# Optimization experiments

Hardware: AMD Instinct MI355X
Metric: run time of the kernel (lower is better)

The kernel has to match this reference:

```python
import jax, jax.numpy as jnp
import numpy as np
import math

B, L, D = 2, 4096, 1024
K = D // 4


def _rotor(angles):
    # angles: [..., 6] -> scalar part s: [...], bivector part: [..., 6]
    mag = jnp.maximum(jnp.linalg.norm(angles, axis=-1), 1e-8)
    s = jnp.cos(mag)
    biv = (jnp.sin(mag) / mag)[..., None] * angles
    return s, biv


def _apply_rotor(s, biv, v):
    # s: [...], biv: [..., 6] (e12,e13,e14,e23,e24,e34), v: [..., 4]
    t12, t13, t14, t23, t24, t34 = (biv[..., i] for i in range(6))
    v1, v2, v3, v4 = (v[..., i] for i in range(4))
    s2 = s * s
    ts = 2.0 * s
    v1n = v1 * (s2 - t12 * t12 - t13 * t13 - t14 * t14) + ts * (v2 * t12 + v3 * t13 + v4 * t14)
    v2n = v2 * (s2 - t12 * t12 - t23 * t23 - t24 * t24) + ts * (-v1 * t12 + v3 * t23 + v4 * t24)
    v3n = v3 * (s2 - t13 * t13 - t23 * t23 - t34 * t34) + ts * (-v1 * t13 - v2 * t23 + v4 * t34)
    v4n = v4 * (s2 - t14 * t14 - t24 * t24 - t34 * t34) + ts * (-v1 * t14 - v2 * t24 - v3 * t34)
    return jnp.stack([v1n, v2n, v3n, v4n], axis=-1)


def _forward(x, wk1, bk1, wk2, bk2, wq1, bq1, wq2, bq2, wv, bv, ln_g, ln_b, wo, bo):
    b, l, d = x.shape
    k = d // 4
    gelu = lambda t: jax.nn.gelu(t, approximate=False)  # torch nn.GELU default = exact
    half_pi = math.pi / 2
    key_angles = (jnp.tanh(gelu(x @ wk1 + bk1) @ wk2 + bk2) * half_pi).reshape(b, l, k, 6)
    query_angles = (jnp.tanh(gelu(x @ wq1 + bq1) @ wq2 + bq2) * half_pi).reshape(b, l, k, 6)
    value = (x @ wv + bv).reshape(b, l, k, 4)
    ks, kb = _rotor(key_angles)
    qs, qb = _rotor(query_angles)
    rotated_value = _apply_rotor(ks, kb, value)          # [B,L,K,4]
    memory = jnp.cumsum(rotated_value, axis=1)            # running sum over sequence
    retrieved = _apply_rotor(qs, -qb, memory)             # reversed query rotor
    retrieved = retrieved.reshape(b, l, d)
    norm = jnp.sqrt(jnp.arange(1, l + 1, dtype=x.dtype))[None, :, None]
    r = retrieved / norm
    # LayerNorm (eps=1e-5) then Linear
    mu = jnp.mean(r, axis=-1, keepdims=True)
    var = jnp.mean((r - mu) ** 2, axis=-1, keepdims=True)
    rn = (r - mu) / jnp.sqrt(var + 1e-5) * ln_g + ln_b
    return x + rn @ wo + bo


def setup_inputs() -> dict:
    key = jax.random.key(0)
    ks = jax.random.split(key, 8)
    lin = lambda k, fi, fo: (jax.random.normal(k, (fi, fo), jnp.float32) * 0.02)
    return {
        "x": jax.random.normal(ks[0], (B, L, D), jnp.float32),
        "wk1": lin(ks[1], D, D), "bk1": jnp.zeros((D,), jnp.float32),
        "wk2": lin(ks[2], D, K * 6), "bk2": jnp.zeros((K * 6,), jnp.float32),
        "wq1": lin(ks[3], D, D), "bq1": jnp.zeros((D,), jnp.float32),
        "wq2": lin(ks[4], D, K * 6), "bq2": jnp.zeros((K * 6,), jnp.float32),
        "wv": lin(ks[5], D, D), "bv": jnp.zeros((D,), jnp.float32),
        "ln_g": jnp.ones((D,), jnp.float32), "ln_b": jnp.zeros((D,), jnp.float32),
        "wo": lin(ks[6], D, D), "bo": jnp.zeros((D,), jnp.float32),
    }


def reference(x, wk1, bk1, wk2, bk2, wq1, bq1, wq2, bq2, wv, bv, ln_g, ln_b, wo, bo):
    return _forward(x, wk1, bk1, wk2, bk2, wq1, bq1, wq2, bq2, wv, bv, ln_g, ln_b, wo, bo)
```

## Files before the change

kernel.cpp:

```cpp
#include <hip/hip_runtime.h>
#include <hip/hip_bf16.h>
#include <math.h>

#define D_DIM 1024
#define L_DIM 4096
#define B_DIM 2
#define K_DIM 256
#define N6    1536
#define M_ROWS 8192
#define CHUNKS 256
#define CHUNK_LEN 16
#define HALF_PI 1.57079632679489662f

typedef __attribute__((ext_vector_type(8))) short short8;
typedef __attribute__((ext_vector_type(4))) float f32x4;
typedef unsigned short us;

__device__ __forceinline__ void gload_lds16(const void* g, void* l) {
    __builtin_amdgcn_global_load_lds(
        (const __attribute__((address_space(1))) unsigned int*)g,
        (__attribute__((address_space(3))) unsigned int*)l,
        16, 0, 0);
}
__device__ __forceinline__ float bf2f(us u) {
    union { unsigned int i; float f; } c; c.i = ((unsigned int)u) << 16; return c.f;
}
__device__ __forceinline__ us f2bf(float v) {
    __hip_bfloat16 h = __float2bfloat16(v);
    return *(us*)&h;
}
__device__ __forceinline__ float tanh_fast(float x) {
    return 1.0f - 2.0f / (1.0f + __expf(2.0f * x));
}
__device__ __forceinline__ float gelu_fast(float x) {
    return x / (1.0f + __expf(-1.5957691216057308f * x * (1.0f + 0.044715f * x * x)));
}

__device__ __forceinline__ void rotor_from_angles(const float a[6], float& s, float b[6]) {
    float m2 = a[0]*a[0] + a[1]*a[1] + a[2]*a[2] + a[3]*a[3] + a[4]*a[4] + a[5]*a[5];
    float mag = fmaxf(sqrtf(m2), 1e-8f);
    s = __cosf(mag);
    float f = __sinf(mag) / mag;
    #pragma unroll
    for (int i = 0; i < 6; ++i) b[i] = f * a[i];
}
__device__ __forceinline__ void apply_rotor(float s, const float b[6], const float v[4], float o[4]) {
    float t12 = b[0], t13 = b[1], t14 = b[2], t23 = b[3], t24 = b[4], t34 = b[5];
    float v1 = v[0], v2 = v[1], v3 = v[2], v4 = v[3];
    float s2 = s * s;
    float ts = 2.0f * s;
    o[0] = v1 * (s2 - t12*t12 - t13*t13 - t14*t14) + ts * ( v2*t12 + v3*t13 + v4*t14);
    o[1] = v2 * (s2 - t12*t12 - t23*t23 - t24*t24) + ts * (-v1*t12 + v3*t23 + v4*t24);
    o[2] = v3 * (s2 - t13*t13 - t23*t23 - t34*t34) + ts * (-v1*t13 - v2*t23 + v4*t34);
    o[3] = v4 * (s2 - t14*t14 - t24*t24 - t34*t34) + ts * (-v1*t14 - v2*t24 - v3*t34);
}

__global__ __launch_bounds__(256)
void pack_b4(const float* __restrict__ w0, const float* __restrict__ w1,
             const float* __restrict__ w2, const float* __restrict__ w3,
             us* __restrict__ o0, us* __restrict__ o1,
             us* __restrict__ o2, us* __restrict__ o3, int Kd, int N)
{
    const float* W = (blockIdx.z == 0) ? w0 : (blockIdx.z == 1) ? w1 : (blockIdx.z == 2) ? w2 : w3;
    us* O = (blockIdx.z == 0) ? o0 : (blockIdx.z == 1) ? o1 : (blockIdx.z == 2) ? o2 : o3;
    if (W == nullptr) return;
    int nf = blockIdx.x;
    int kt = blockIdx.y * 4 + (threadIdx.x >> 6);
    int l = threadIdx.x & 63;
    int n = nf * 16 + (l & 15);
    int k0 = kt * 32 + (l >> 4) * 8;
    union { us u[8]; uint4 v; } pk;
    #pragma unroll
    for (int j = 0; j < 8; ++j)
        pk.u[j] = f2bf(W[(size_t)(k0 + j) * N + n]);
    *(uint4*)(O + ((size_t)nf * (Kd >> 5) + kt) * 512 + l * 8) = pk.v;
}

__global__ __launch_bounds__(256)
void cvt_bf16_kernel(const float* __restrict__ in, us* __restrict__ out)
{
    size_t i = ((size_t)blockIdx.x * 256 + threadIdx.x) * 8;
    float4 v0 = *(const float4*)(in + i);
    float4 v1 = *(const float4*)(in + i + 4);
    union { us u[8]; uint4 v; } pk;
    pk.u[0] = f2bf(v0.x); pk.u[1] = f2bf(v0.y); pk.u[2] = f2bf(v0.z); pk.u[3] = f2bf(v0.w);
    pk.u[4] = f2bf(v1.x); pk.u[5] = f2bf(v1.y); pk.u[6] = f2bf(v1.z); pk.u[7] = f2bf(v1.w);
    *(uint4*)(out + i) = pk.v;
}

__device__ __forceinline__ int xcd_swz(int bid, int nwg) {
    int cpx = nwg >> 3;
    return (bid & 7) * cpx + (bid >> 3);
}


#define GBAR()  do { __builtin_amdgcn_s_barrier(); __builtin_amdgcn_sched_barrier(0); } while (0)

__device__ __forceinline__ void gemm128_core(
    const us* __restrict__ Ab, const us* __restrict__ Bp, int Kd, int bn,
    short* lds, f32x4 (&acc)[4][4])
{
    const int tid = threadIdx.x;
    const int l = tid & 63, w = tid >> 6;
    const int wr = w >> 1, wc = w & 1;
    const int fr = l & 15, fq = l >> 4;
    const int nkt = Kd >> 5;

    #pragma unroll
    for (int i = 0; i < 4; ++i)
        #pragma unroll
        for (int j = 0; j < 4; ++j)
            acc[i][j] = (f32x4){0.f, 0.f, 0.f, 0.f};

    const us* bptr[4];
    #pragma unroll
    for (int ni = 0; ni < 4; ++ni)
        bptr[ni] = Bp + ((size_t)((bn >> 4) + wc * 4 + ni) * nkt) * 512 + l * 8;

    const int sr = tid >> 2, su = tid & 3;
    const int slu = su ^ ((sr >> 1) & 3);
    const us* gA0 = Ab + (size_t)sr * Kd + slu * 8;
    const us* gA1 = gA0 + (size_t)64 * Kd;

    const int swu = (fq ^ ((fr >> 1) & 3)) * 8;
    const int arow = (wr * 64 + fr) * 32 + swu;

    gload_lds16(gA0,      lds + tid * 8);
    gload_lds16(gA1,      lds + 2048 + tid * 8);
    gload_lds16(gA0 + 32, lds + 4096 + tid * 8);
    gload_lds16(gA1 + 32, lds + 6144 + tid * 8);
    gload_lds16(gA0 + 64, lds + 8192 + tid * 8);
    gload_lds16(gA1 + 64, lds + 10240 + tid * 8);
    short8 bcur[4], bnxt[4];
    #pragma unroll
    for (int ni = 0; ni < 4; ++ni)
        bcur[ni] = *(const short8*)(bptr[ni]);
    asm volatile("s_waitcnt vmcnt(8)" ::: "memory");
    GBAR();

    #pragma unroll 2
    for (int t = 0; t < nkt; ++t) {
        const int cb = (t % 3) * 4096;
        const int sb = ((t + 2) % 3) * 4096;
        const int ka = ((t + 2) < nkt ? (t + 2) : (nkt - 1)) * 32;
        const int kb = ((t + 1) < nkt ? (t + 1) : (nkt - 1));

        #pragma unroll
        for (int ni = 0; ni < 4; ++ni)
            bnxt[ni] = *(const short8*)(bptr[ni] + (size_t)kb * 512);
        gload_lds16(gA0 + ka, lds + sb + tid * 8);
        gload_lds16(gA1 + ka, lds + sb + 2048 + tid * 8);

        short8 a[4];
        #pragma unroll
        for (int mi = 0; mi < 4; ++mi)
            a[mi] = *(const short8*)(lds + cb + arow + mi * 512);

        __builtin_amdgcn_s_setprio(1);
        #pragma unroll
        for (int mi = 0; mi < 4; ++mi)
            #pragma unroll
            for (int ni = 0; ni < 4; ++ni)
                acc[mi][ni] = __builtin_amdgcn_mfma_f32_16x16x32_bf16(bcur[ni], a[mi], acc[mi][ni], 0, 0, 0);
        __builtin_amdgcn_sched_barrier(0);
        __builtin_amdgcn_s_setprio(0);

        #pragma unroll
        for (int ni = 0; ni < 4; ++ni)
            bcur[ni] = bnxt[ni];

        asm volatile("s_waitcnt vmcnt(6)" ::: "memory");
        GBAR();
    }
}

__global__ __launch_bounds__(256, 3)
void gemm_fused3(const us* __restrict__ xb,
                 const us* __restrict__ w0p, const us* __restrict__ w1p, const us* __restrict__ w2p,
                 const float* __restrict__ b0, const float* __restrict__ b1, const float* __restrict__ b2,
                 us* __restrict__ o0, us* __restrict__ o1, us* __restrict__ o2)
{
    __shared__ short lds[12288];
    const int wg = xcd_swz(blockIdx.x, 1536);
    const int bm = (wg / 24) * 128;
    const int col = wg % 24;
    const int r = col >> 3;
    const int bn = (col & 7) * 128;
    const us* Bp = (r == 0) ? w0p : (r == 1) ? w1p : w2p;
    const float* bias = (r == 0) ? b0 : (r == 1) ? b1 : b2;
    us* outp = (r == 0) ? o0 : (r == 1) ? o1 : o2;
    f32x4 acc[4][4];
    gemm128_core(xb + (size_t)bm * D_DIM, Bp, D_DIM, bn, lds, acc);
    const int l = threadIdx.x & 63, w = threadIdx.x >> 6;
    const int wr = w >> 1, wc = w & 1, fr = l & 15, fq = l >> 4;
    #pragma unroll
    for (int mi = 0; mi < 4; ++mi) {
        int row = bm + wr * 64 + mi * 16 + fr;
        #pragma unroll
        for (int ni = 0; ni < 4; ++ni) {
            int c0 = bn + wc * 64 + ni * 16 + fq * 4;
            float4 bs = *(const float4*)(bias + c0);
            float v0 = acc[mi][ni][0] + bs.x, v1 = acc[mi][ni][1] + bs.y;
            float v2 = acc[mi][ni][2] + bs.z, v3 = acc[mi][ni][3] + bs.w;
            if (r < 2) { v0 = gelu_fast(v0); v1 = gelu_fast(v1); v2 = gelu_fast(v2); v3 = gelu_fast(v3); }
            ushort4 pk; pk.x = f2bf(v0); pk.y = f2bf(v1); pk.z = f2bf(v2); pk.w = f2bf(v3);
            *(ushort4*)(outp + (size_t)row * D_DIM + c0) = pk;
        }
    }
}

__global__ __launch_bounds__(256, 3)
void gemm_angles(const us* __restrict__ Hk, const us* __restrict__ Hq,
                 const us* __restrict__ wk2p, const us* __restrict__ wq2p,
                 const float* __restrict__ bk2, const float* __restrict__ bq2,
                 us* __restrict__ ak, us* __restrict__ aq)
{
    __shared__ short lds[12288];
    const int wg = xcd_swz(blockIdx.x, 1536);
    const int z = wg / 768;
    const int rem = wg % 768;
    const int bm = (rem / 12) * 128;
    const int bn = (rem % 12) * 128;
    const us* A  = z ? Hq : Hk;
    const us* Bp = z ? wq2p : wk2p;
    const float* bias = z ? bq2 : bk2;
    us* outp = z ? aq : ak;
    f32x4 acc[4][4];
    gemm128_core(A + (size_t)bm * D_DIM, Bp, D_DIM, bn, lds, acc);
    const int l = threadIdx.x & 63, w = threadIdx.x >> 6;
    const int wr = w >> 1, wc = w & 1, fr = l & 15, fq = l >> 4;
    #pragma unroll
    for (int mi = 0; mi < 4; ++mi) {
        int row = bm + wr * 64 + mi * 16 + fr;
        #pragma unroll
        for (int ni = 0; ni < 4; ++ni) {
            int c0 = bn + wc * 64 + ni * 16 + fq * 4;
            float4 bs = *(const float4*)(bias + c0);
            ushort4 pk;
            pk.x = f2bf(tanh_fast(acc[mi][ni][0] + bs.x) * HALF_PI);
            pk.y = f2bf(tanh_fast(acc[mi][ni][1] + bs.y) * HALF_PI);
            pk.z = f2bf(tanh_fast(acc[mi][ni][2] + bs.z) * HALF_PI);
            pk.w = f2bf(tanh_fast(acc[mi][ni][3] + bs.w) * HALF_PI);
            *(ushort4*)(outp + (size_t)row * N6 + c0) = pk;
        }
    }
}

__global__ __launch_bounds__(256, 3)
void gemm_final(const us* __restrict__ rn, const us* __restrict__ wop,
                const float* __restrict__ bo, const float* __restrict__ x,
                float* __restrict__ out)
{
    __shared__ short lds[12288];
    const int wg = xcd_swz(blockIdx.x, 512);
    const int bm = (wg / 8) * 128;
    const int bn = (wg % 8) * 128;
    f32x4 acc[4][4];
    gemm128_core(rn + (size_t)bm * D_DIM, wop, D_DIM, bn, lds, acc);
    const int l = threadIdx.x & 63, w = threadIdx.x >> 6;
    const int wr = w >> 1, wc = w & 1, fr = l & 15, fq = l >> 4;
    #pragma unroll
    for (int mi = 0; mi < 4; ++mi) {
        int row = bm + wr * 64 + mi * 16 + fr;
        #pragma unroll
        for (int ni = 0; ni < 4; ++ni) {
            int c0 = bn + wc * 64 + ni * 16 + fq * 4;
            size_t off = (size_t)row * D_DIM + c0;
            float4 bs = *(const float4*)(bo + c0);
            float4 rx = *(const float4*)(x + off);
            float4 o;
            o.x = acc[mi][ni][0] + bs.x + rx.x;
            o.y = acc[mi][ni][1] + bs.y + rx.y;
            o.z = acc[mi][ni][2] + bs.z + rx.z;
            o.w = acc[mi][ni][3] + bs.w + rx.w;
            *(float4*)(out + off) = o;
        }
    }
}

__global__ __launch_bounds__(256)
void rot_chunk_sum(const us* __restrict__ value, const us* __restrict__ ak,
                   float4* __restrict__ sums)
{
    int bc = blockIdx.x;
    int b = bc >> 8, c = bc & 255;
    int k = threadIdx.x;
    float4 acc = make_float4(0.f, 0.f, 0.f, 0.f);
    size_t row0 = (size_t)b * L_DIM + c * CHUNK_LEN;
    for (int i = 0; i < CHUNK_LEN; ++i) {
        size_t row = row0 + i;
        ushort4 uv = *(const ushort4*)(value + row * D_DIM + k * 4);
        const unsigned int* ap = (const unsigned int*)(ak + row * N6 + k * 6);
        unsigned int a0 = ap[0], a1 = ap[1], a2 = ap[2];
        float a[6] = { bf2f(a0 & 0xffff), bf2f(a0 >> 16), bf2f(a1 & 0xffff),
                       bf2f(a1 >> 16), bf2f(a2 & 0xffff), bf2f(a2 >> 16) };
        float s, bb[6];
        rotor_from_angles(a, s, bb);
        float v[4] = {bf2f(uv.x), bf2f(uv.y), bf2f(uv.z), bf2f(uv.w)}, o[4];
        apply_rotor(s, bb, v, o);
        acc.x += o[0]; acc.y += o[1]; acc.z += o[2]; acc.w += o[3];
    }
    sums[(size_t)bc * 256 + k] = acc;
}

__global__ __launch_bounds__(256)
void scan_chunks_kernel(const float4* __restrict__ sums, float4* __restrict__ carry)
{
    int b = blockIdx.x >> 8;
    int k = blockIdx.x & 255;
    int c = threadIdx.x;
    __shared__ float4 sh[CHUNKS];
    float4 v = sums[((size_t)(b * CHUNKS + c)) * 256 + k];
    sh[c] = v;
    __syncthreads();
    for (int off = 1; off < CHUNKS; off <<= 1) {
        float4 t = make_float4(0.f, 0.f, 0.f, 0.f);
        if (c >= off) t = sh[c - off];
        __syncthreads();
        v.x += t.x; v.y += t.y; v.z += t.z; v.w += t.w;
        sh[c] = v;
        __syncthreads();
    }
    float4 ex = make_float4(0.f, 0.f, 0.f, 0.f);
    if (c > 0) ex = sh[c - 1];
    carry[((size_t)(b * CHUNKS + c)) * 256 + k] = ex;
}

__global__ __launch_bounds__(256)
void scan_apply_ln(const us* __restrict__ value, const us* __restrict__ ak,
                   const us* __restrict__ aq, const float4* __restrict__ carry,
                   const float* __restrict__ g, const float* __restrict__ bta,
                   us* __restrict__ rn)
{
    int bc = blockIdx.x;
    int b = bc >> 8, c = bc & 255;
    int k = threadIdx.x;
    int wv = k >> 6, lane = k & 63;
    float4 run = carry[(size_t)bc * 256 + k];
    float4 gv = *(const float4*)(g + k * 4);
    float4 bv = *(const float4*)(bta + k * 4);
    __shared__ float reds[4], redq[4];
    for (int i = 0; i < CHUNK_LEN; ++i) {
        int l = c * CHUNK_LEN + i;
        size_t row = (size_t)b * L_DIM + l;
        ushort4 uv = *(const ushort4*)(value + row * D_DIM + k * 4);
        const unsigned int* akp = (const unsigned int*)(ak + row * N6 + k * 6);
        unsigned int ka0 = akp[0], ka1 = akp[1], ka2 = akp[2];
        float a[6] = { bf2f(ka0 & 0xffff), bf2f(ka0 >> 16), bf2f(ka1 & 0xffff),
                       bf2f(ka1 >> 16), bf2f(ka2 & 0xffff), bf2f(ka2 >> 16) };
        float s, bb[6];
        rotor_from_angles(a, s, bb);
        float v[4] = {bf2f(uv.x), bf2f(uv.y), bf2f(uv.z), bf2f(uv.w)}, o[4];
        apply_rotor(s, bb, v, o);
        run.x += o[0]; run.y += o[1]; run.z += o[2]; run.w += o[3];
        const unsigned int* aqp = (const unsigned int*)(aq + row * N6 + k * 6);
        unsigned int qa0 = aqp[0], qa1 = aqp[1], qa2 = aqp[2];
        float aq6[6] = { bf2f(qa0 & 0xffff), bf2f(qa0 >> 16), bf2f(qa1 & 0xffff),
                         bf2f(qa1 >> 16), bf2f(qa2 & 0xffff), bf2f(qa2 >> 16) };
        float qs, qb[6];
        rotor_from_angles(aq6, qs, qb);
        #pragma unroll
        for (int t = 0; t < 6; ++t) qb[t] = -qb[t];
        float mem[4] = {run.x, run.y, run.z, run.w}, o2[4];
        apply_rotor(qs, qb, mem, o2);
        float inv = rsqrtf((float)(l + 1));
        o2[0] *= inv; o2[1] *= inv; o2[2] *= inv; o2[3] *= inv;
        float sm = o2[0] + o2[1] + o2[2] + o2[3];
        float qm = o2[0]*o2[0] + o2[1]*o2[1] + o2[2]*o2[2] + o2[3]*o2[3];
        #pragma unroll
        for (int off = 1; off < 64; off <<= 1) {
            sm += __shfl_xor(sm, off);
            qm += __shfl_xor(qm, off);
        }
        if (lane == 0) { reds[wv] = sm; redq[wv] = qm; }
        __syncthreads();
        sm = reds[0] + reds[1] + reds[2] + reds[3];
        qm = redq[0] + redq[1] + redq[2] + redq[3];
        float mu = sm * (1.0f / 1024.0f);
        float var = qm * (1.0f / 1024.0f) - mu * mu;
        float rstd = rsqrtf(var + 1e-5f);
        ushort4 pk;
        pk.x = f2bf((o2[0] - mu) * rstd * gv.x + bv.x);
        pk.y = f2bf((o2[1] - mu) * rstd * gv.y + bv.y);
        pk.z = f2bf((o2[2] - mu) * rstd * gv.z + bv.z);
        pk.w = f2bf((o2[3] - mu) * rstd * gv.w + bv.w);
        *(ushort4*)(rn + row * D_DIM + k * 4) = pk;
        __syncthreads();
    }
}

extern "C" void kernel_launch(void* const* d_in, const int* in_sizes, int n_in,
                              void* d_out, int out_size, void* d_ws, size_t ws_size,
                              hipStream_t stream)
{
    const float* x   = (const float*)d_in[0];
    const float* wk1 = (const float*)d_in[1];
    const float* bk1 = (const float*)d_in[2];
    const float* wk2 = (const float*)d_in[3];
    const float* bk2 = (const float*)d_in[4];
    const float* wq1 = (const float*)d_in[5];
    const float* bq1 = (const float*)d_in[6];
    const float* wq2 = (const float*)d_in[7];
    const float* bq2 = (const float*)d_in[8];
    const float* wv  = (const float*)d_in[9];
    const float* bv  = (const float*)d_in[10];
    const float* lng = (const float*)d_in[11];
    const float* lnb = (const float*)d_in[12];
    const float* wo  = (const float*)d_in[13];
    const float* bo  = (const float*)d_in[14];
    float* out = (float*)d_out;

    char* ws = (char*)d_ws;
    us* xb    = (us*)(ws);
    us* Hk    = (us*)(ws + (16ull  << 20));
    us* Hq    = (us*)(ws + (32ull  << 20));
    us* val   = (us*)(ws + (48ull  << 20));
    us* ak    = (us*)(ws + (64ull  << 20));
    us* aq    = (us*)(ws + (88ull  << 20));
    float4* sums  = (float4*)(ws + (112ull << 20));
    float4* carry = (float4*)(ws + (114ull << 20));
    us* wk1p  = (us*)(ws + (116ull << 20));
    us* wq1p  = (us*)(ws + (118ull << 20));
    us* wvp   = (us*)(ws + (120ull << 20));
    us* wop   = (us*)(ws + (122ull << 20));
    us* wk2p  = (us*)(ws + (124ull << 20));
    us* wq2p  = (us*)(ws + (127ull << 20));
    us* rn    = xb;

    dim3 blk(256);
    pack_b4<<<dim3(D_DIM / 16, D_DIM / 128, 4), blk, 0, stream>>>(
        wk1, wq1, wv, wo, wk1p, wq1p, wvp, wop, D_DIM, D_DIM);
    pack_b4<<<dim3(N6 / 16, D_DIM / 128, 2), blk, 0, stream>>>(
        wk2, wq2, nullptr, nullptr, wk2p, wq2p, nullptr, nullptr, D_DIM, N6);
    cvt_bf16_kernel<<<dim3(M_ROWS * D_DIM / (256 * 8)), blk, 0, stream>>>(x, xb);

    gemm_fused3<<<dim3(1536), blk, 0, stream>>>(
        xb, wk1p, wq1p, wvp, bk1, bq1, bv, Hk, Hq, val);
    gemm_angles<<<dim3(1536), blk, 0, stream>>>(
        Hk, Hq, wk2p, wq2p, bk2, bq2, ak, aq);
    rot_chunk_sum<<<dim3(B_DIM * CHUNKS), blk, 0, stream>>>(val, ak, sums);
    scan_chunks_kernel<<<dim3(B_DIM * K_DIM), blk, 0, stream>>>(sums, carry);
    scan_apply_ln<<<dim3(B_DIM * CHUNKS), blk, 0, stream>>>(val, ak, aq, carry, lng, lnb, rn);
    gemm_final<<<dim3(512), blk, 0, stream>>>(rn, wop, bo, x, out);
}
```

Baseline: 242.6 us.

## Load GEMM A operand directly from global into registers, dropping LDS staging

The shared GEMM core no longer stages A tiles in LDS with async global-to-LDS loads and barriers. Each wave now reads its A and B fragments straight from global memory into registers, double-buffered over two k-steps. This removes the LDS traffic and block-wide barriers, but A rows are now loaded redundantly by the two column waves. The per-lane strided 16-byte loads across rows also coalesce less well and put more load on L2.

```diff
diff --git a/kernel.cpp b/kernel.cpp
--- a/kernel.cpp
+++ b/kernel.cpp
@@ -16,12 +16,6 @@
 typedef __attribute__((ext_vector_type(4))) float f32x4;
 typedef unsigned short us;
 
-__device__ __forceinline__ void gload_lds16(const void* g, void* l) {
-    __builtin_amdgcn_global_load_lds(
-        (const __attribute__((address_space(1))) unsigned int*)g,
-        (__attribute__((address_space(3))) unsigned int*)l,
-        16, 0, 0);
-}
 __device__ __forceinline__ float bf2f(us u) {
     union { unsigned int i; float f; } c; c.i = ((unsigned int)u) << 16; return c.f;
 }
@@ -94,11 +88,9 @@
 }
 
 
-#define GBAR()  do { __builtin_amdgcn_s_barrier(); __builtin_amdgcn_sched_barrier(0); } while (0)
-
 __device__ __forceinline__ void gemm128_core(
     const us* __restrict__ Ab, const us* __restrict__ Bp, int Kd, int bn,
-    short* lds, f32x4 (&acc)[4][4])
+    f32x4 (&acc)[4][4])
 {
     const int tid = threadIdx.x;
     const int l = tid & 63, w = tid >> 6;
@@ -112,65 +104,48 @@
         for (int j = 0; j < 4; ++j)
             acc[i][j] = (f32x4){0.f, 0.f, 0.f, 0.f};
 
+    const us* aptr[4];
+    #pragma unroll
+    for (int mi = 0; mi < 4; ++mi)
+        aptr[mi] = Ab + (size_t)(wr * 64 + mi * 16 + fr) * Kd + fq * 8;
     const us* bptr[4];
     #pragma unroll
     for (int ni = 0; ni < 4; ++ni)
         bptr[ni] = Bp + ((size_t)((bn >> 4) + wc * 4 + ni) * nkt) * 512 + l * 8;
 
-    const int sr = tid >> 2, su = tid & 3;
-    const int slu = su ^ ((sr >> 1) & 3);
-    const us* gA0 = Ab + (size_t)sr * Kd + slu * 8;
-    const us* gA1 = gA0 + (size_t)64 * Kd;
-
-    const int swu = (fq ^ ((fr >> 1) & 3)) * 8;
-    const int arow = (wr * 64 + fr) * 32 + swu;
-
-    gload_lds16(gA0,      lds + tid * 8);
-    gload_lds16(gA1,      lds + 2048 + tid * 8);
-    gload_lds16(gA0 + 32, lds + 4096 + tid * 8);
-    gload_lds16(gA1 + 32, lds + 6144 + tid * 8);
-    gload_lds16(gA0 + 64, lds + 8192 + tid * 8);
-    gload_lds16(gA1 + 64, lds + 10240 + tid * 8);
-    short8 bcur[4], bnxt[4];
-    #pragma unroll
-    for (int ni = 0; ni < 4; ++ni)
-        bcur[ni] = *(const short8*)(bptr[ni]);
-    asm volatile("s_waitcnt vmcnt(8)" ::: "memory");
-    GBAR();
-
-    #pragma unroll 2
-    for (int t = 0; t < nkt; ++t) {
-        const int cb = (t % 3) * 4096;
-        const int sb = ((t + 2) % 3) * 4096;
-        const int ka = ((t + 2) < nkt ? (t + 2) : (nkt - 1)) * 32;
-        const int kb = ((t + 1) < nkt ? (t + 1) : (nkt - 1));
-
-        #pragma unroll
-        for (int ni = 0; ni < 4; ++ni)
-            bnxt[ni] = *(const short8*)(bptr[ni] + (size_t)kb * 512);
-        gload_lds16(gA0 + ka, lds + sb + tid * 8);
-        gload_lds16(gA1 + ka, lds + sb + 2048 + tid * 8);
-
-        short8 a[4];
-        #pragma unroll
-        for (int mi = 0; mi < 4; ++mi)
-            a[mi] = *(const short8*)(lds + cb + arow + mi * 512);
-
+    short8 a0[4], b0[4], a1[4], b1[4];
+    #pragma unroll
+    for (int i = 0; i < 4; ++i) {
+        a0[i] = *(const short8*)(aptr[i]);
+        b0[i] = *(const short8*)(bptr[i]);
+    }
+
+    for (int t = 0; t < nkt; t += 2) {
+        #pragma unroll
+        for (int i = 0; i < 4; ++i) {
+            a1[i] = *(const short8*)(aptr[i] + (t + 1) * 32);
+            b1[i] = *(const short8*)(bptr[i] + (size_t)(t + 1) * 512);
+        }
         __builtin_amdgcn_s_setprio(1);
         #pragma unroll
         for (int mi = 0; mi < 4; ++mi)
             #pragma unroll
             for (int ni = 0; ni < 4; ++ni)
-                acc[mi][ni] = __builtin_amdgcn_mfma_f32_16x16x32_bf16(bcur[ni], a[mi], acc[mi][ni], 0, 0, 0);
-        __builtin_amdgcn_sched_barrier(0);
+                acc[mi][ni] = __builtin_amdgcn_mfma_f32_16x16x32_bf16(b0[ni], a0[mi], acc[mi][ni], 0, 0, 0);
         __builtin_amdgcn_s_setprio(0);
-
-        #pragma unroll
-        for (int ni = 0; ni < 4; ++ni)
-            bcur[ni] = bnxt[ni];
-
-        asm volatile("s_waitcnt vmcnt(6)" ::: "memory");
-        GBAR();
+        const int t2 = (t + 2 < nkt) ? (t + 2) : (nkt - 1);
+        #pragma unroll
+        for (int i = 0; i < 4; ++i) {
+            a0[i] = *(const short8*)(aptr[i] + t2 * 32);
+            b0[i] = *(const short8*)(bptr[i] + (size_t)t2 * 512);
+        }
+        __builtin_amdgcn_s_setprio(1);
+        #pragma unroll
+        for (int mi = 0; mi < 4; ++mi)
+            #pragma unroll
+            for (int ni = 0; ni < 4; ++ni)
+                acc[mi][ni] = __builtin_amdgcn_mfma_f32_16x16x32_bf16(b1[ni], a1[mi], acc[mi][ni], 0, 0, 0);
+        __builtin_amdgcn_s_setprio(0);
     }
 }
 
@@ -180,7 +155,6 @@
                  const float* __restrict__ b0, const float* __restrict__ b1, const float* __restrict__ b2,
                  us* __restrict__ o0, us* __restrict__ o1, us* __restrict__ o2)
 {
-    __shared__ short lds[12288];
     const int wg = xcd_swz(blockIdx.x, 1536);
     const int bm = (wg / 24) * 128;
     const int col = wg % 24;
@@ -190,7 +164,7 @@
     const float* bias = (r == 0) ? b0 : (r == 1) ? b1 : b2;
     us* outp = (r == 0) ? o0 : (r == 1) ? o1 : o2;
     f32x4 acc[4][4];
-    gemm128_core(xb + (size_t)bm * D_DIM, Bp, D_DIM, bn, lds, acc);
+    gemm128_core(xb + (size_t)bm * D_DIM, Bp, D_DIM, bn, acc);
     const int l = threadIdx.x & 63, w = threadIdx.x >> 6;
     const int wr = w >> 1, wc = w & 1, fr = l & 15, fq = l >> 4;
     #pragma unroll
@@ -215,7 +189,6 @@
                  const float* __restrict__ bk2, const float* __restrict__ bq2,
                  us* __restrict__ ak, us* __restrict__ aq)
 {
-    __shared__ short lds[12288];
     const int wg = xcd_swz(blockIdx.x, 1536);
     const int z = wg / 768;
     const int rem = wg % 768;
@@ -226,7 +199,7 @@
     const float* bias = z ? bq2 : bk2;
     us* outp = z ? aq : ak;
     f32x4 acc[4][4];
-    gemm128_core(A + (size_t)bm * D_DIM, Bp, D_DIM, bn, lds, acc);
+    gemm128_core(A + (size_t)bm * D_DIM, Bp, D_DIM, bn, acc);
     const int l = threadIdx.x & 63, w = threadIdx.x >> 6;
     const int wr = w >> 1, wc = w & 1, fr = l & 15, fq = l >> 4;
     #pragma unroll
@@ -251,12 +224,11 @@
                 const float* __restrict__ bo, const float* __restrict__ x,
                 float* __restrict__ out)
 {
-    __shared__ short lds[12288];
     const int wg = xcd_swz(blockIdx.x, 512);
     const int bm = (wg / 8) * 128;
     const int bn = (wg % 8) * 128;
     f32x4 acc[4][4];
-    gemm128_core(rn + (size_t)bm * D_DIM, wop, D_DIM, bn, lds, acc);
+    gemm128_core(rn + (size_t)bm * D_DIM, wop, D_DIM, bn, acc);
     const int l = threadIdx.x & 63, w = threadIdx.x >> 6;
     const int wr = w >> 1, wc = w & 1, fr = l & 15, fq = l >> 4;
     #pragma unroll
```

After: 358.2 us. +47.6%, slower.

## Store rotated values in chunk-sum pass and double-buffer B fragments in GEMM

Applied to the files above, without the earlier changes.

rot_chunk_sum now writes the key-rotated value back to the value buffer in bf16, so scan_apply_ln no longer reads key angles or recomputes the key rotor and only accumulates the stored rotated values. The shared GEMM mainloop is manually unrolled by two with ping-pong B register sets, so B loads for the step after next are issued after the MFMAs instead of copying bnxt to bcur each step. The extra bf16 rounding of the rotated values slightly changes numerics. The unroll-by-two loop assumes an even number of K tiles.

```diff
diff --git a/kernel.cpp b/kernel.cpp
--- a/kernel.cpp
+++ b/kernel.cpp
@@ -131,46 +131,64 @@
     gload_lds16(gA1 + 32, lds + 6144 + tid * 8);
     gload_lds16(gA0 + 64, lds + 8192 + tid * 8);
     gload_lds16(gA1 + 64, lds + 10240 + tid * 8);
-    short8 bcur[4], bnxt[4];
-    #pragma unroll
-    for (int ni = 0; ni < 4; ++ni)
-        bcur[ni] = *(const short8*)(bptr[ni]);
-    asm volatile("s_waitcnt vmcnt(8)" ::: "memory");
+    asm volatile("s_waitcnt vmcnt(4)" ::: "memory");
+    short8 bA[4], bB[4];
+    #pragma unroll
+    for (int ni = 0; ni < 4; ++ni) bA[ni] = *(const short8*)(bptr[ni]);
+    #pragma unroll
+    for (int ni = 0; ni < 4; ++ni) bB[ni] = *(const short8*)(bptr[ni] + 512);
     GBAR();
 
-    #pragma unroll 2
-    for (int t = 0; t < nkt; ++t) {
-        const int cb = (t % 3) * 4096;
-        const int sb = ((t + 2) % 3) * 4096;
-        const int ka = ((t + 2) < nkt ? (t + 2) : (nkt - 1)) * 32;
-        const int kb = ((t + 1) < nkt ? (t + 1) : (nkt - 1));
-
-        #pragma unroll
-        for (int ni = 0; ni < 4; ++ni)
-            bnxt[ni] = *(const short8*)(bptr[ni] + (size_t)kb * 512);
-        gload_lds16(gA0 + ka, lds + sb + tid * 8);
-        gload_lds16(gA1 + ka, lds + sb + 2048 + tid * 8);
-
-        short8 a[4];
-        #pragma unroll
-        for (int mi = 0; mi < 4; ++mi)
-            a[mi] = *(const short8*)(lds + cb + arow + mi * 512);
-
-        __builtin_amdgcn_s_setprio(1);
-        #pragma unroll
-        for (int mi = 0; mi < 4; ++mi)
+    for (int t = 0; t < nkt; t += 2) {
+        {
+            const int cb = (t % 3) * 4096;
+            const int sb = ((t + 2) % 3) * 4096;
+            const int tp = (t + 2 < nkt) ? (t + 2) : (nkt - 1);
+            short8 a[4];
+            #pragma unroll
+            for (int mi = 0; mi < 4; ++mi)
+                a[mi] = *(const short8*)(lds + cb + arow + mi * 512);
+            gload_lds16(gA0 + tp * 32, lds + sb + tid * 8);
+            gload_lds16(gA1 + tp * 32, lds + sb + 2048 + tid * 8);
+            __builtin_amdgcn_s_setprio(1);
+            #pragma unroll
+            for (int mi = 0; mi < 4; ++mi)
+                #pragma unroll
+                for (int ni = 0; ni < 4; ++ni)
+                    acc[mi][ni] = __builtin_amdgcn_mfma_f32_16x16x32_bf16(bA[ni], a[mi], acc[mi][ni], 0, 0, 0);
+            __builtin_amdgcn_sched_barrier(0);
+            __builtin_amdgcn_s_setprio(0);
             #pragma unroll
             for (int ni = 0; ni < 4; ++ni)
-                acc[mi][ni] = __builtin_amdgcn_mfma_f32_16x16x32_bf16(bcur[ni], a[mi], acc[mi][ni], 0, 0, 0);
-        __builtin_amdgcn_sched_barrier(0);
-        __builtin_amdgcn_s_setprio(0);
-
-        #pragma unroll
-        for (int ni = 0; ni < 4; ++ni)
-            bcur[ni] = bnxt[ni];
-
-        asm volatile("s_waitcnt vmcnt(6)" ::: "memory");
-        GBAR();
+                bA[ni] = *(const short8*)(bptr[ni] + (size_t)tp * 512);
+            asm volatile("s_waitcnt vmcnt(6)" ::: "memory");
+            GBAR();
+        }
+        {
+            const int t1 = t + 1;
+            const int cb = (t1 % 3) * 4096;
+            const int sb = ((t1 + 2) % 3) * 4096;
+            const int tp = (t1 + 2 < nkt) ? (t1 + 2) : (nkt - 1);
+            short8 a[4];
+            #pragma unroll
+            for (int mi = 0; mi < 4; ++mi)
+                a[mi] = *(const short8*)(lds + cb + arow + mi * 512);
+            gload_lds16(gA0 + tp * 32, lds + sb + tid * 8);
+            gload_lds16(gA1 + tp * 32, lds + sb + 2048 + tid * 8);
+            __builtin_amdgcn_s_setprio(1);
+            #pragma unroll
+            for (int mi = 0; mi < 4; ++mi)
+                #pragma unroll
+                for (int ni = 0; ni < 4; ++ni)
+                    acc[mi][ni] = __builtin_amdgcn_mfma_f32_16x16x32_bf16(bB[ni], a[mi], acc[mi][ni], 0, 0, 0);
+            __builtin_amdgcn_sched_barrier(0);
+            __builtin_amdgcn_s_setprio(0);
+            #pragma unroll
+            for (int ni = 0; ni < 4; ++ni)
+                bB[ni] = *(const short8*)(bptr[ni] + (size_t)tp * 512);
+            asm volatile("s_waitcnt vmcnt(6)" ::: "memory");
+            GBAR();
+        }
     }
 }
 
@@ -279,7 +297,7 @@
 }
 
 __global__ __launch_bounds__(256)
-void rot_chunk_sum(const us* __restrict__ value, const us* __restrict__ ak,
+void rot_chunk_sum(us* __restrict__ value, const us* __restrict__ ak,
                    float4* __restrict__ sums)
 {
     int bc = blockIdx.x;
@@ -298,7 +316,10 @@
         rotor_from_angles(a, s, bb);
         float v[4] = {bf2f(uv.x), bf2f(uv.y), bf2f(uv.z), bf2f(uv.w)}, o[4];
         apply_rotor(s, bb, v, o);
-        acc.x += o[0]; acc.y += o[1]; acc.z += o[2]; acc.w += o[3];
+        ushort4 pkr;
+        pkr.x = f2bf(o[0]); pkr.y = f2bf(o[1]); pkr.z = f2bf(o[2]); pkr.w = f2bf(o[3]);
+        *(ushort4*)(value + row * D_DIM + k * 4) = pkr;
+        acc.x += bf2f(pkr.x); acc.y += bf2f(pkr.y); acc.z += bf2f(pkr.z); acc.w += bf2f(pkr.w);
     }
     sums[(size_t)bc * 256 + k] = acc;
 }
@@ -327,8 +348,8 @@
 }
 
 __global__ __launch_bounds__(256)
-void scan_apply_ln(const us* __restrict__ value, const us* __restrict__ ak,
-                   const us* __restrict__ aq, const float4* __restrict__ carry,
+void scan_apply_ln(const us* __restrict__ value, const us* __restrict__ aq,
+                   const float4* __restrict__ carry,
                    const float* __restrict__ g, const float* __restrict__ bta,
                    us* __restrict__ rn)
 {
@@ -344,15 +365,7 @@
         int l = c * CHUNK_LEN + i;
         size_t row = (size_t)b * L_DIM + l;
         ushort4 uv = *(const ushort4*)(value + row * D_DIM + k * 4);
-        const unsigned int* akp = (const unsigned int*)(ak + row * N6 + k * 6);
-        unsigned int ka0 = akp[0], ka1 = akp[1], ka2 = akp[2];
-        float a[6] = { bf2f(ka0 & 0xffff), bf2f(ka0 >> 16), bf2f(ka1 & 0xffff),
-                       bf2f(ka1 >> 16), bf2f(ka2 & 0xffff), bf2f(ka2 >> 16) };
-        float s, bb[6];
-        rotor_from_angles(a, s, bb);
-        float v[4] = {bf2f(uv.x), bf2f(uv.y), bf2f(uv.z), bf2f(uv.w)}, o[4];
-        apply_rotor(s, bb, v, o);
-        run.x += o[0]; run.y += o[1]; run.z += o[2]; run.w += o[3];
+        run.x += bf2f(uv.x); run.y += bf2f(uv.y); run.z += bf2f(uv.z); run.w += bf2f(uv.w);
         const unsigned int* aqp = (const unsigned int*)(aq + row * N6 + k * 6);
         unsigned int qa0 = aqp[0], qa1 = aqp[1], qa2 = aqp[2];
         float aq6[6] = { bf2f(qa0 & 0xffff), bf2f(qa0 >> 16), bf2f(qa1 & 0xffff),
@@ -440,6 +453,6 @@
         Hk, Hq, wk2p, wq2p, bk2, bq2, ak, aq);
     rot_chunk_sum<<<dim3(B_DIM * CHUNKS), blk, 0, stream>>>(val, ak, sums);
     scan_chunks_kernel<<<dim3(B_DIM * K_DIM), blk, 0, stream>>>(sums, carry);
-    scan_apply_ln<<<dim3(B_DIM * CHUNKS), blk, 0, stream>>>(val, ak, aq, carry, lng, lnb, rn);
+    scan_apply_ln<<<dim3(B_DIM * CHUNKS), blk, 0, stream>>>(val, aq, carry, lng, lnb, rn);
     gemm_final<<<dim3(512), blk, 0, stream>>>(rn, wop, bo, x, out);
 }
```

Measured after the change: 229.3 us. -5.5%, faster.
